# Kernel tuning notes

Hardware: AMD Instinct MI355X
Metric: run time of the kernel (lower is better)

## Reference

```python
import jax, jax.numpy as jnp
import numpy as np

EPS = 1e-5  # torch BatchNorm2d default eps
K = 3       # kernel_size
D = 1       # dilation (== padding)


def setup_inputs() -> dict:
    key = jax.random.key(0)
    k0, k1, k2 = jax.random.split(key, 3)
    N, C, H, W, O = 4, 2048, 32, 32, 256
    return {
        "x": jax.random.normal(k0, (N, C, H, W), jnp.float32),
        "conv_w": jax.random.normal(k1, (K * K, C, K, K), jnp.float32) * 0.01,
        "gamma": jnp.ones((K * K,), jnp.float32),
        "beta": jnp.zeros((K * K,), jnp.float32),
        "weight": jax.random.normal(k2, (O, C, K * K), jnp.float32) * 0.01,
    }


def reference(x, conv_w, gamma, beta, weight):
    n, c, h, w = x.shape
    # --- dynamic-kernel generator: conv (stride 1, pad=dilation) -> BN (train mode) -> softmax over K*K ---
    sigma = jax.lax.conv_general_dilated(
        x, conv_w, window_strides=(1, 1), padding=[(D, D), (D, D)],
        rhs_dilation=(D, D), dimension_numbers=("NCHW", "OIHW", "NCHW"))  # (n, K*K, h, w)
    mean = sigma.mean(axis=(0, 2, 3), keepdims=True)
    var = sigma.var(axis=(0, 2, 3), keepdims=True)  # biased variance, as torch BN uses for normalization
    sigma = (sigma - mean) * jax.lax.rsqrt(var + EPS)
    sigma = sigma * gamma[None, :, None, None] + beta[None, :, None, None]
    sigma = jax.nn.softmax(sigma, axis=1)            # softmax over the K*K kernel positions
    sigma = sigma.reshape(n, K * K, h * w)           # (n, K*K, h*w)
    # --- unfold (im2col), channel-major (C, kh, kw) ordering matching torch F.unfold ---
    patches = jax.lax.conv_general_dilated_patches(
        x, (K, K), (1, 1), [(D, D), (D, D)], rhs_dilation=(D, D),
        dimension_numbers=("NCHW", "OIHW", "NCHW"))  # (n, C*K*K, h, w)
    patches = patches.reshape(n, c, K * K, h * w)     # (n, C, K*K, h*w)
    # --- per-pixel dynamic weighting + learned projection ---
    # out[n,o,m] = sum_{c,l} patches[n,c,l,m] * sigma[n,l,m] * weight[o,c,l]
    out = jnp.einsum("nclm,nlm,ocl->nom", patches, sigma, weight)
    return out.reshape(n, weight.shape[0], h, w)
```

## Files before the change

kernel.cpp:

```cpp
#include <hip/hip_runtime.h>
#include <hip/hip_bf16.h>
#include <stdint.h>

typedef unsigned short u16;
typedef __attribute__((ext_vector_type(8))) short short8;
typedef __attribute__((ext_vector_type(4))) float floatx4;

#define N_IMG 4
#define C_IN  2048
#define HW    1024
#define KK    9
#define O_OUT 256
#define NPIX  4096
#define M_PAD  2560
#define H_ROWS 2432
#define K_DIM  2048
#define BN_EPS 1e-5f

#define OFF_A    0u
#define OFF_XT   10485760u
#define OFF_H    27262976u
#define OFF_SRAW 47185920u
#define OFF_STAT 47333376u

__device__ __forceinline__ u16 f2b(float f) {
    unsigned u = __float_as_uint(f);
    return (u16)((u + 0x7FFFu + ((u >> 16) & 1u)) >> 16);
}

__device__ __forceinline__ void load8f(const float* base, size_t eidx, u16* out) {
    const float* p = base + eidx;
    float4 a = ((const float4*)p)[0];
    float4 b = ((const float4*)p)[1];
    float f[8] = {a.x, a.y, a.z, a.w, b.x, b.y, b.z, b.w};
#pragma unroll
    for (int j = 0; j < 8; ++j) out[j] = f2b(f[j]);
}

__global__ void build_all(const float* __restrict__ x, const float* __restrict__ wgt,
                          const float* __restrict__ cw, u16* __restrict__ xt,
                          u16* __restrict__ A, float* __restrict__ stats) {
    __shared__ __align__(16) u16 lds[9 * 2056];
    int b = blockIdx.x, t = threadIdx.x;
    if (b < 2048) {
        int c0 = (b & 31) * 64, p0 = ((b >> 5) & 15) * 64, n = b >> 9;
        int rp = t >> 3;
        int pv = (t & 7) * 8;
        u16 h0[8], h1[8];
        load8f(x, (size_t)(n * C_IN + c0 + 2 * rp) * HW + p0 + pv, h0);
        load8f(x, (size_t)(n * C_IN + c0 + 2 * rp + 1) * HW + p0 + pv, h1);
        unsigned* l32 = (unsigned*)lds;
#pragma unroll
        for (int j = 0; j < 8; ++j)
            l32[(pv + j) * 35 + rp] = (unsigned)h0[j] | ((unsigned)h1[j] << 16);
        __syncthreads();
        int pr = t >> 3, cq = (t & 7) * 4;
        unsigned o0[4], o1[4];
#pragma unroll
        for (int i = 0; i < 4; ++i) {
            o0[i] = l32[pr * 35 + cq + i];
            o1[i] = l32[(pr + 32) * 35 + cq + i];
        }
        *(uint4*)(xt + (size_t)(n * HW + p0 + pr) * K_DIM + c0 + cq * 2) = *(uint4*)o0;
        *(uint4*)(xt + (size_t)(n * HW + p0 + pr + 32) * K_DIM + c0 + cq * 2) = *(uint4*)o1;
    } else if (b < 2304) {
        int o = b - 2048;
        size_t base = (size_t)o * 18432;
        for (int i = 0; i < 9; ++i) {
            int e0 = (t + i * 256) * 8;
            u16 hv[8];
            load8f(wgt, base + e0, hv);
#pragma unroll
            for (int j = 0; j < 8; ++j) {
                int e = e0 + j;
                int c = e / 9, l = e - c * 9;
                lds[l * 2056 + c] = hv[j];
            }
        }
        __syncthreads();
        for (int l = 0; l < 9; ++l) {
            size_t row = (size_t)l * 256 + o;
            *(uint4*)(A + row * K_DIM + t * 8) = *(const uint4*)&lds[l * 2056 + t * 8];
        }
    } else if (b < 2313) {
        int l = b - 2304;
        size_t base = (size_t)l * 18432;
        for (int i = 0; i < 9; ++i) {
            int e0 = (t + i * 256) * 8;
            u16 hv[8];
            load8f(cw, base + e0, hv);
#pragma unroll
            for (int j = 0; j < 8; ++j) {
                int e = e0 + j;
                int c = e / 9, k = e - c * 9;
                lds[k * 2056 + c] = hv[j];
            }
        }
        __syncthreads();
        for (int k = 0; k < 9; ++k) {
            size_t row = 2304 + (size_t)k * 9 + l;
            *(uint4*)(A + row * K_DIM + t * 8) = *(const uint4*)&lds[k * 2056 + t * 8];
        }
    } else {
        uint4 z = {0, 0, 0, 0};
        uint4* dst = (uint4*)(A + (size_t)2385 * K_DIM);
        for (int i = t; i < (47 * 2048) / 8; i += 256) dst[i] = z;
        if (t < 18) stats[t] = 0.0f;
    }
}

__device__ __forceinline__ void gload_lds16(const void* g, void* l) {
    __builtin_amdgcn_global_load_lds((__attribute__((address_space(1))) void*)(g),
                                     (__attribute__((address_space(3))) void*)(l), 16, 0, 0);
}

#define STG_A(bb, kt) do {                                                                   \
    gload_lds16(gA0 + (size_t)(w * 8) * K_DIM + (size_t)(kt) * 64,                           \
                As + (bb) * 10240 + w * 512);                                                \
    gload_lds16(gA0 + (size_t)((w + 8) * 8) * K_DIM + (size_t)(kt) * 64,                     \
                As + (bb) * 10240 + (w + 8) * 512);                                          \
    if (w < 4)                                                                               \
        gload_lds16(gA0 + (size_t)((w + 16) * 8) * K_DIM + (size_t)(kt) * 64,                \
                    As + (bb) * 10240 + (w + 16) * 512);                                     \
} while (0)

#define STG_B(bb, hh, kt) do {                                                               \
    gload_lds16(gB0 + (size_t)((hh) * 128 + (w * 2 + 0) * 8) * K_DIM + (size_t)(kt) * 64,    \
                Bs + (bb) * 16384 + (hh) * 8192 + w * 1024);                                 \
    gload_lds16(gB0 + (size_t)((hh) * 128 + (w * 2 + 1) * 8) * K_DIM + (size_t)(kt) * 64,    \
                Bs + (bb) * 16384 + (hh) * 8192 + w * 1024 + 512);                           \
} while (0)

#define RD_A(bb, mi, ks) (*(const short8*)(As + (bb) * 10240 + arow + (mi) * 1024 + col[ks]))
#define RD_B(bb, ni, ks) (*(const short8*)(Bs + (bb) * 16384 + brow + (ni) * 1024 + col[ks]))

#define READ_BALL(bb) do {                                                   \
    bq[0][0] = RD_B(bb, 0, 0); bq[1][0] = RD_B(bb, 1, 0);                    \
    bq[2][0] = RD_B(bb, 2, 0); bq[3][0] = RD_B(bb, 3, 0);                    \
    bq[0][1] = RD_B(bb, 0, 1); bq[1][1] = RD_B(bb, 1, 1);                    \
    bq[2][1] = RD_B(bb, 2, 1); bq[3][1] = RD_B(bb, 3, 1);                    \
} while (0)

#define READ_A2(bb, mlo, mhi) do {                                           \
    aq[0][0] = RD_A(bb, mlo, 0); aq[1][0] = RD_A(bb, mhi, 0);                \
    aq[0][1] = RD_A(bb, mlo, 1); aq[1][1] = RD_A(bb, mhi, 1);                \
} while (0)

#define READ_A1(bb, m) do {                                                  \
    aq[0][0] = RD_A(bb, m, 0); aq[0][1] = RD_A(bb, m, 1);                    \
} while (0)

#define MF(a, b, c) __builtin_amdgcn_mfma_f32_16x16x32_bf16(a, b, c, 0, 0, 0)

#define MFMA_PAIR(mlo, mhi) do {                                                             \
    acc[mlo][0] = MF(aq[0][0], bq[0][0], acc[mlo][0]); acc[mhi][0] = MF(aq[1][0], bq[0][0], acc[mhi][0]); \
    acc[mlo][1] = MF(aq[0][0], bq[1][0], acc[mlo][1]); acc[mhi][1] = MF(aq[1][0], bq[1][0], acc[mhi][1]); \
    acc[mlo][2] = MF(aq[0][0], bq[2][0], acc[mlo][2]); acc[mhi][2] = MF(aq[1][0], bq[2][0], acc[mhi][2]); \
    acc[mlo][3] = MF(aq[0][0], bq[3][0], acc[mlo][3]); acc[mhi][3] = MF(aq[1][0], bq[3][0], acc[mhi][3]); \
    acc[mlo][0] = MF(aq[0][1], bq[0][1], acc[mlo][0]); acc[mhi][0] = MF(aq[1][1], bq[0][1], acc[mhi][0]); \
    acc[mlo][1] = MF(aq[0][1], bq[1][1], acc[mlo][1]); acc[mhi][1] = MF(aq[1][1], bq[1][1], acc[mhi][1]); \
    acc[mlo][2] = MF(aq[0][1], bq[2][1], acc[mlo][2]); acc[mhi][2] = MF(aq[1][1], bq[2][1], acc[mhi][2]); \
    acc[mlo][3] = MF(aq[0][1], bq[3][1], acc[mlo][3]); acc[mhi][3] = MF(aq[1][1], bq[3][1], acc[mhi][3]); \
} while (0)

#define MFMA_ONE(m) do {                                                                     \
    acc[m][0] = MF(aq[0][0], bq[0][0], acc[m][0]); acc[m][1] = MF(aq[0][0], bq[1][0], acc[m][1]); \
    acc[m][2] = MF(aq[0][0], bq[2][0], acc[m][2]); acc[m][3] = MF(aq[0][0], bq[3][0], acc[m][3]); \
    acc[m][0] = MF(aq[0][1], bq[0][1], acc[m][0]); acc[m][1] = MF(aq[0][1], bq[1][1], acc[m][1]); \
    acc[m][2] = MF(aq[0][1], bq[2][1], acc[m][2]); acc[m][3] = MF(aq[0][1], bq[3][1], acc[m][3]); \
} while (0)

#define FENCE() asm volatile("" ::: "memory")
#define BARRIER() do { FENCE(); __builtin_amdgcn_s_barrier(); FENCE(); } while (0)

#define BAR1_PAIR(mlo, mhi) do {                             \
    BARRIER();                                               \
    __builtin_amdgcn_s_setprio(1);                           \
    MFMA_PAIR(mlo, mhi);                                     \
    __builtin_amdgcn_s_setprio(0);                           \
} while (0)
#define BAR1_ONE(m) do {                                     \
    BARRIER();                                               \
    __builtin_amdgcn_s_setprio(1);                           \
    MFMA_ONE(m);                                             \
    __builtin_amdgcn_s_setprio(0);                           \
} while (0)
#define VMW4() asm volatile("s_waitcnt vmcnt(4)" ::: "memory")
#define VMW0() asm volatile("s_waitcnt vmcnt(0)" ::: "memory")

__global__ __launch_bounds__(512, 2) void gemm_bt(const u16* __restrict__ A,
                                                  const u16* __restrict__ B,
                                                  __hip_bfloat16* __restrict__ C) {
    __shared__ __align__(16) u16 As[2 * 160 * 64];
    __shared__ __align__(16) u16 Bs[2 * 256 * 64];

    int orig = blockIdx.x;
    int wgid = (orig & 7) * 32 + (orig >> 3);
    int nt = wgid >> 4, mt = wgid & 15;
    int m0 = mt * 160, n0 = nt * 256;

    int t = threadIdx.x;
    int w = t >> 6, L = t & 63;
    int wm = w >> 2, wn = w & 3;
    int q = L >> 4, lm = L & 15;
    int lr = L >> 3, ls = L & 7;

    int csw = (ls ^ lr) * 8;
    const u16* gA0 = A + (size_t)(m0 + lr) * K_DIM + csw;
    const u16* gB0 = B + (size_t)(n0 + lr) * K_DIM + csw;

    int sw = (lm & 7) << 3;
    int arow = (wm * 80 + lm) * 64;
    int brow = (wn * 64 + lm) * 64;
    int col[2] = { (q * 8) ^ sw, (32 + q * 8) ^ sw };

    floatx4 acc[5][4];
    floatx4 z = {0.f, 0.f, 0.f, 0.f};
#pragma unroll
    for (int i = 0; i < 5; ++i)
#pragma unroll
        for (int j = 0; j < 4; ++j) acc[i][j] = z;

    short8 aq[2][2], bq[4][2];

    STG_A(0, 0);
    STG_B(0, 0, 0); STG_B(0, 1, 0);
    STG_B(1, 0, 1); STG_B(1, 1, 1);
    VMW4();
    BARRIER();

    for (int it = 0; it < 15; ++it) {
        int T = 2 * it;
        READ_A2(0, 0, 1); READ_BALL(0);
        STG_A(1, T + 1);
        BAR1_PAIR(0, 1);
        BARRIER();
        READ_A2(0, 2, 3);
        STG_B(0, 0, T + 2);
        BAR1_PAIR(2, 3);
        READ_A1(0, 4);
        STG_B(0, 1, T + 2);
        BAR1_ONE(4);
        VMW4(); BARRIER();
        READ_A2(1, 0, 1); READ_BALL(1);
        STG_A(0, T + 2);
        BAR1_PAIR(0, 1);
        BARRIER();
        READ_A2(1, 2, 3);
        STG_B(1, 0, T + 3);
        BAR1_PAIR(2, 3);
        READ_A1(1, 4);
        STG_B(1, 1, T + 3);
        BAR1_ONE(4);
        VMW4(); BARRIER();
    }

    READ_A2(0, 0, 1); READ_BALL(0);
    STG_A(1, 31);
    BAR1_PAIR(0, 1);
    READ_A2(0, 2, 3); BAR1_PAIR(2, 3);
    READ_A1(0, 4);    BAR1_ONE(4);
    VMW0(); BARRIER();
    READ_A2(1, 0, 1); READ_BALL(1); BAR1_PAIR(0, 1);
    READ_A2(1, 2, 3); BAR1_PAIR(2, 3);
    READ_A1(1, 4);    BAR1_ONE(4);

    if (m0 + 159 < H_ROWS) {
#pragma unroll
        for (int mi = 0; mi < 5; ++mi) {
            int gm = m0 + wm * 80 + mi * 16 + q * 4;
#pragma unroll
            for (int ni = 0; ni < 4; ++ni) {
                int gn = n0 + wn * 64 + ni * 16 + lm;
#pragma unroll
                for (int r = 0; r < 4; ++r)
                    C[(size_t)(gm + r) * NPIX + gn] = __float2bfloat16(acc[mi][ni][r]);
            }
        }
    } else {
#pragma unroll
        for (int mi = 0; mi < 5; ++mi) {
            int gm = m0 + wm * 80 + mi * 16 + q * 4;
#pragma unroll
            for (int ni = 0; ni < 4; ++ni) {
                int gn = n0 + wn * 64 + ni * 16 + lm;
#pragma unroll
                for (int r = 0; r < 4; ++r) {
                    int row = gm + r;
                    if (row < H_ROWS)
                        C[(size_t)row * NPIX + gn] = __float2bfloat16(acc[mi][ni][r]);
                }
            }
        }
    }
}

__global__ void sigma_stats(const __hip_bfloat16* __restrict__ Hm, float* __restrict__ sraw,
                            float* __restrict__ stats) {
    int b = blockIdx.x;
    int qq = b & 3, nl = b >> 2;
    int n = nl / 9, l = nl - n * 9;
    int t = threadIdx.x;
    int pix = qq * 256 + t;
    int y = pix >> 5, x = pix & 31;
    float v = 0.f;
#pragma unroll
    for (int k = 0; k < 9; ++k) {
        int yy = y + k / 3 - 1, xx = x + (k % 3) - 1;
        if (yy >= 0 && yy < 32 && xx >= 0 && xx < 32)
            v += __bfloat162float(Hm[(size_t)(2304 + k * 9 + l) * NPIX + n * HW + yy * 32 + xx]);
    }
    sraw[(size_t)nl * HW + pix] = v;
    __shared__ float r1[256], r2[256];
    r1[t] = v; r2[t] = v * v;
    __syncthreads();
    for (int s = 128; s > 0; s >>= 1) {
        if (t < s) { r1[t] += r1[t + s]; r2[t] += r2[t + s]; }
        __syncthreads();
    }
    if (t == 0) { atomicAdd(&stats[l], r1[0]); atomicAdd(&stats[9 + l], r2[0]); }
}

__global__ void tail(const __hip_bfloat16* __restrict__ Hm, const float* __restrict__ sraw,
                     const float* __restrict__ stats, const float* __restrict__ gamma,
                     const float* __restrict__ beta, float* __restrict__ out) {
    int b = blockIdx.x;
    int n = b >> 8, rem = b & 255;
    int ph = rem >> 7, og = rem & 127;
    int t = threadIdx.x;
    float mean[9], istd[9], gg[9], bb[9];
#pragma unroll
    for (int l = 0; l < 9; ++l) {
        float m = stats[l] * (1.f / 4096.f);
        float var = stats[9 + l] * (1.f / 4096.f) - m * m;
        mean[l] = m; istd[l] = rsqrtf(var + BN_EPS);
        gg[l] = gamma[l]; bb[l] = beta[l];
    }
    const __hip_bfloat16* hb = Hm + (size_t)(og * 2) * NPIX + (size_t)n * HW;
    float* ob = out + ((size_t)n * 256 + og * 2) * HW;
#pragma unroll
    for (int i = 0; i < 2; ++i) {
        int pix = ph * 512 + i * 256 + t;
        int y = pix >> 5, x = pix & 31;
        float v[9];
        float mx = -1e30f;
#pragma unroll
        for (int l = 0; l < 9; ++l) {
            float tv = (sraw[(size_t)(n * 9 + l) * HW + pix] - mean[l]) * istd[l];
            tv = tv * gg[l] + bb[l];
            v[l] = tv; mx = fmaxf(mx, tv);
        }
        float ssum = 0.f;
#pragma unroll
        for (int l = 0; l < 9; ++l) { v[l] = __expf(v[l] - mx); ssum += v[l]; }
        float inv = 1.f / ssum;
        float acc0 = 0.f, acc1 = 0.f;
#pragma unroll
        for (int l = 0; l < 9; ++l) {
            int dy = l / 3 - 1, dx = l % 3 - 1;
            int yy = y + dy, xx = x + dx;
            if (yy >= 0 && yy < 32 && xx >= 0 && xx < 32) {
                float sv = v[l] * inv;
                size_t hidx = (size_t)(l * 256) * NPIX + (size_t)(pix + dy * 32 + dx);
                acc0 += sv * __bfloat162float(hb[hidx]);
                acc1 += sv * __bfloat162float(hb[hidx + NPIX]);
            }
        }
        ob[pix] = acc0;
        ob[HW + pix] = acc1;
    }
}

extern "C" void kernel_launch(void* const* d_in, const int* in_sizes, int n_in,
                              void* d_out, int out_size, void* d_ws, size_t ws_size,
                              hipStream_t stream) {
    const float* x     = (const float*)d_in[0];
    const float* cw    = (const float*)d_in[1];
    const float* gamma = (const float*)d_in[2];
    const float* beta  = (const float*)d_in[3];
    const float* wgt   = (const float*)d_in[4];

    char* ws = (char*)d_ws;
    u16*   Abuf = (u16*)(ws + OFF_A);
    u16*   XT   = (u16*)(ws + OFF_XT);
    u16*   Hm   = (u16*)(ws + OFF_H);
    float* sraw = (float*)(ws + OFF_SRAW);
    float* stats= (float*)(ws + OFF_STAT);

    build_all<<<2314, 256, 0, stream>>>(x, wgt, cw, XT, Abuf, stats);
    gemm_bt<<<256, 512, 0, stream>>>(Abuf, XT, (__hip_bfloat16*)Hm);
    sigma_stats<<<N_IMG * KK * 4, 256, 0, stream>>>((const __hip_bfloat16*)Hm, sraw, stats);
    tail<<<1024, 256, 0, stream>>>((const __hip_bfloat16*)Hm, sraw, stats, gamma, beta, (float*)d_out);
}
```

Measured before the change: 159.8 us.

## Software-pipeline LDS fragment reads ahead of MFMA groups in GEMM main loop

Restructures the GEMM inner loop so that LDS fragment reads for the next MFMA group are issued before the current group's MFMAs. The MFMA work is regrouped into three phases (a 2x2 block, a cross block, and the rest) that reuse fragments already in registers. The next tile's first fragments are prefetched into a double-buffered register set before the buffer flip. This is meant to hide LDS read latency behind matrix work, at the cost of more live VGPRs and changed waitcnt/barrier placement (vmcnt(2) instead of vmcnt(4)).

```diff
diff --git a/kernel.cpp b/kernel.cpp
--- a/kernel.cpp
+++ b/kernel.cpp
@@ -134,57 +134,66 @@
 #define RD_A(bb, mi, ks) (*(const short8*)(As + (bb) * 10240 + arow + (mi) * 1024 + col[ks]))
 #define RD_B(bb, ni, ks) (*(const short8*)(Bs + (bb) * 16384 + brow + (ni) * 1024 + col[ks]))
 
-#define READ_BALL(bb) do {                                                   \
-    bq[0][0] = RD_B(bb, 0, 0); bq[1][0] = RD_B(bb, 1, 0);                    \
-    bq[2][0] = RD_B(bb, 2, 0); bq[3][0] = RD_B(bb, 3, 0);                    \
-    bq[0][1] = RD_B(bb, 0, 1); bq[1][1] = RD_B(bb, 1, 1);                    \
-    bq[2][1] = RD_B(bb, 2, 1); bq[3][1] = RD_B(bb, 3, 1);                    \
-} while (0)
-
-#define READ_A2(bb, mlo, mhi) do {                                           \
-    aq[0][0] = RD_A(bb, mlo, 0); aq[1][0] = RD_A(bb, mhi, 0);                \
-    aq[0][1] = RD_A(bb, mlo, 1); aq[1][1] = RD_A(bb, mhi, 1);                \
-} while (0)
-
-#define READ_A1(bb, m) do {                                                  \
-    aq[0][0] = RD_A(bb, m, 0); aq[0][1] = RD_A(bb, m, 1);                    \
+#define PRE_S0(par, bb) do {                                                 \
+    s0A[par][0][0] = RD_A(bb, 0, 0); s0A[par][1][0] = RD_A(bb, 1, 0);        \
+    s0B[par][0][0] = RD_B(bb, 0, 0); s0B[par][1][0] = RD_B(bb, 1, 0);        \
+    s0A[par][0][1] = RD_A(bb, 0, 1); s0A[par][1][1] = RD_A(bb, 1, 1);        \
+    s0B[par][0][1] = RD_B(bb, 0, 1); s0B[par][1][1] = RD_B(bb, 1, 1);        \
+} while (0)
+
+#define PRE_S1(bb) do {                                                      \
+    s1A[0][0] = RD_A(bb, 2, 0); s1A[1][0] = RD_A(bb, 3, 0);                  \
+    s1B[0][0] = RD_B(bb, 2, 0); s1B[1][0] = RD_B(bb, 3, 0);                  \
+    s1A[0][1] = RD_A(bb, 2, 1); s1A[1][1] = RD_A(bb, 3, 1);                  \
+    s1B[0][1] = RD_B(bb, 2, 1); s1B[1][1] = RD_B(bb, 3, 1);                  \
+} while (0)
+
+#define PRE_S2(bb) do {                                                      \
+    s2A[0] = RD_A(bb, 4, 0); s2A[1] = RD_A(bb, 4, 1);                        \
 } while (0)
 
 #define MF(a, b, c) __builtin_amdgcn_mfma_f32_16x16x32_bf16(a, b, c, 0, 0, 0)
 
-#define MFMA_PAIR(mlo, mhi) do {                                                             \
-    acc[mlo][0] = MF(aq[0][0], bq[0][0], acc[mlo][0]); acc[mhi][0] = MF(aq[1][0], bq[0][0], acc[mhi][0]); \
-    acc[mlo][1] = MF(aq[0][0], bq[1][0], acc[mlo][1]); acc[mhi][1] = MF(aq[1][0], bq[1][0], acc[mhi][1]); \
-    acc[mlo][2] = MF(aq[0][0], bq[2][0], acc[mlo][2]); acc[mhi][2] = MF(aq[1][0], bq[2][0], acc[mhi][2]); \
-    acc[mlo][3] = MF(aq[0][0], bq[3][0], acc[mlo][3]); acc[mhi][3] = MF(aq[1][0], bq[3][0], acc[mhi][3]); \
-    acc[mlo][0] = MF(aq[0][1], bq[0][1], acc[mlo][0]); acc[mhi][0] = MF(aq[1][1], bq[0][1], acc[mhi][0]); \
-    acc[mlo][1] = MF(aq[0][1], bq[1][1], acc[mlo][1]); acc[mhi][1] = MF(aq[1][1], bq[1][1], acc[mhi][1]); \
-    acc[mlo][2] = MF(aq[0][1], bq[2][1], acc[mlo][2]); acc[mhi][2] = MF(aq[1][1], bq[2][1], acc[mhi][2]); \
-    acc[mlo][3] = MF(aq[0][1], bq[3][1], acc[mlo][3]); acc[mhi][3] = MF(aq[1][1], bq[3][1], acc[mhi][3]); \
-} while (0)
-
-#define MFMA_ONE(m) do {                                                                     \
-    acc[m][0] = MF(aq[0][0], bq[0][0], acc[m][0]); acc[m][1] = MF(aq[0][0], bq[1][0], acc[m][1]); \
-    acc[m][2] = MF(aq[0][0], bq[2][0], acc[m][2]); acc[m][3] = MF(aq[0][0], bq[3][0], acc[m][3]); \
-    acc[m][0] = MF(aq[0][1], bq[0][1], acc[m][0]); acc[m][1] = MF(aq[0][1], bq[1][1], acc[m][1]); \
-    acc[m][2] = MF(aq[0][1], bq[2][1], acc[m][2]); acc[m][3] = MF(aq[0][1], bq[3][1], acc[m][3]); \
-} while (0)
+#define G0K(par, k) do {                                                     \
+    acc[0][0] = MF(s0A[par][0][k], s0B[par][0][k], acc[0][0]);               \
+    acc[0][1] = MF(s0A[par][0][k], s0B[par][1][k], acc[0][1]);               \
+    acc[1][0] = MF(s0A[par][1][k], s0B[par][0][k], acc[1][0]);               \
+    acc[1][1] = MF(s0A[par][1][k], s0B[par][1][k], acc[1][1]);               \
+} while (0)
+#define G0(par) do { G0K(par, 0); G0K(par, 1); } while (0)
+
+#define G1K(par, k) do {                                                     \
+    acc[0][2] = MF(s0A[par][0][k], s1B[0][k], acc[0][2]);                    \
+    acc[0][3] = MF(s0A[par][0][k], s1B[1][k], acc[0][3]);                    \
+    acc[1][2] = MF(s0A[par][1][k], s1B[0][k], acc[1][2]);                    \
+    acc[1][3] = MF(s0A[par][1][k], s1B[1][k], acc[1][3]);                    \
+    acc[2][0] = MF(s1A[0][k], s0B[par][0][k], acc[2][0]);                    \
+    acc[2][1] = MF(s1A[0][k], s0B[par][1][k], acc[2][1]);                    \
+    acc[3][0] = MF(s1A[1][k], s0B[par][0][k], acc[3][0]);                    \
+    acc[3][1] = MF(s1A[1][k], s0B[par][1][k], acc[3][1]);                    \
+} while (0)
+#define G1(par) do { G1K(par, 0); G1K(par, 1); } while (0)
+
+#define G2K(par, k) do {                                                     \
+    acc[2][2] = MF(s1A[0][k], s1B[0][k], acc[2][2]);                         \
+    acc[2][3] = MF(s1A[0][k], s1B[1][k], acc[2][3]);                         \
+    acc[3][2] = MF(s1A[1][k], s1B[0][k], acc[3][2]);                         \
+    acc[3][3] = MF(s1A[1][k], s1B[1][k], acc[3][3]);                         \
+    acc[4][0] = MF(s2A[k], s0B[par][0][k], acc[4][0]);                       \
+    acc[4][1] = MF(s2A[k], s0B[par][1][k], acc[4][1]);                       \
+    acc[4][2] = MF(s2A[k], s1B[0][k], acc[4][2]);                           \
+    acc[4][3] = MF(s2A[k], s1B[1][k], acc[4][3]);                           \
+} while (0)
+#define G2(par) do { G2K(par, 0); G2K(par, 1); } while (0)
 
 #define FENCE() asm volatile("" ::: "memory")
 #define BARRIER() do { FENCE(); __builtin_amdgcn_s_barrier(); FENCE(); } while (0)
-
-#define BAR1_PAIR(mlo, mhi) do {                             \
-    BARRIER();                                               \
+#define PRIO_MFMA(GRP) do {                                  \
     __builtin_amdgcn_s_setprio(1);                           \
-    MFMA_PAIR(mlo, mhi);                                     \
+    GRP;                                                     \
     __builtin_amdgcn_s_setprio(0);                           \
 } while (0)
-#define BAR1_ONE(m) do {                                     \
-    BARRIER();                                               \
-    __builtin_amdgcn_s_setprio(1);                           \
-    MFMA_ONE(m);                                             \
-    __builtin_amdgcn_s_setprio(0);                           \
-} while (0)
+#define VMW2() asm volatile("s_waitcnt vmcnt(2)" ::: "memory")
 #define VMW4() asm volatile("s_waitcnt vmcnt(4)" ::: "memory")
 #define VMW0() asm volatile("s_waitcnt vmcnt(0)" ::: "memory")
 
@@ -221,49 +230,63 @@
 #pragma unroll
         for (int j = 0; j < 4; ++j) acc[i][j] = z;
 
-    short8 aq[2][2], bq[4][2];
+    short8 s0A[2][2][2], s0B[2][2][2];
+    short8 s1A[2][2], s1B[2][2];
+    short8 s2A[2];
 
     STG_A(0, 0);
     STG_B(0, 0, 0); STG_B(0, 1, 0);
     STG_B(1, 0, 1); STG_B(1, 1, 1);
     VMW4();
     BARRIER();
+    PRE_S0(0, 0);
 
     for (int it = 0; it < 15; ++it) {
         int T = 2 * it;
-        READ_A2(0, 0, 1); READ_BALL(0);
+        BARRIER();
+        PRE_S1(0);
         STG_A(1, T + 1);
-        BAR1_PAIR(0, 1);
+        PRIO_MFMA(G0(0));
         BARRIER();
-        READ_A2(0, 2, 3);
+        PRE_S2(0);
         STG_B(0, 0, T + 2);
-        BAR1_PAIR(2, 3);
-        READ_A1(0, 4);
+        PRIO_MFMA(G1(0));
+        VMW2(); BARRIER();
+        PRE_S0(1, 1);
         STG_B(0, 1, T + 2);
-        BAR1_ONE(4);
-        VMW4(); BARRIER();
-        READ_A2(1, 0, 1); READ_BALL(1);
+        PRIO_MFMA(G2(0));
+        BARRIER();
+        PRE_S1(1);
         STG_A(0, T + 2);
-        BAR1_PAIR(0, 1);
+        PRIO_MFMA(G0(1));
         BARRIER();
-        READ_A2(1, 2, 3);
+        PRE_S2(1);
         STG_B(1, 0, T + 3);
-        BAR1_PAIR(2, 3);
-        READ_A1(1, 4);
+        PRIO_MFMA(G1(1));
+        VMW2(); BARRIER();
+        PRE_S0(0, 0);
         STG_B(1, 1, T + 3);
-        BAR1_ONE(4);
-        VMW4(); BARRIER();
-    }
-
-    READ_A2(0, 0, 1); READ_BALL(0);
+        PRIO_MFMA(G2(1));
+    }
+
+    BARRIER();
+    PRE_S1(0);
     STG_A(1, 31);
-    BAR1_PAIR(0, 1);
-    READ_A2(0, 2, 3); BAR1_PAIR(2, 3);
-    READ_A1(0, 4);    BAR1_ONE(4);
+    PRIO_MFMA(G0(0));
+    BARRIER();
+    PRE_S2(0);
+    PRIO_MFMA(G1(0));
     VMW0(); BARRIER();
-    READ_A2(1, 0, 1); READ_BALL(1); BAR1_PAIR(0, 1);
-    READ_A2(1, 2, 3); BAR1_PAIR(2, 3);
-    READ_A1(1, 4);    BAR1_ONE(4);
+    PRE_S0(1, 1);
+    PRIO_MFMA(G2(0));
+    BARRIER();
+    PRE_S1(1);
+    PRIO_MFMA(G0(1));
+    BARRIER();
+    PRE_S2(1);
+    PRIO_MFMA(G1(1));
+    BARRIER();
+    PRIO_MFMA(G2(1));
 
     if (m0 + 159 < H_ROWS) {
 #pragma unroll
```

After: 162.6 us. Within noise of the previous version (+1.8%).

## Load GEMM A operand directly from global into registers, bypassing LDS

Applied to the files above, without the earlier changes.

Drops the LDS staging buffer for the A tile. Each wave now loads its own A fragments from global memory straight into a double-buffered register array, while B is still staged through LDS. The per-k-step schedule is cut from several barrier-separated MFMA groups to one compute block per buffer. This removes LDS traffic and barriers for A, but raises register pressure (20 extra short8 per thread) under launch bounds of 512 threads at 2 blocks per SM. It also relies on uncoalesced, duplicated global reads of A across waves that share the same rows.

```diff
diff --git a/kernel.cpp b/kernel.cpp
--- a/kernel.cpp
+++ b/kernel.cpp
@@ -114,16 +114,6 @@
                                      (__attribute__((address_space(3))) void*)(l), 16, 0, 0);
 }
 
-#define STG_A(bb, kt) do {                                                                   \
-    gload_lds16(gA0 + (size_t)(w * 8) * K_DIM + (size_t)(kt) * 64,                           \
-                As + (bb) * 10240 + w * 512);                                                \
-    gload_lds16(gA0 + (size_t)((w + 8) * 8) * K_DIM + (size_t)(kt) * 64,                     \
-                As + (bb) * 10240 + (w + 8) * 512);                                          \
-    if (w < 4)                                                                               \
-        gload_lds16(gA0 + (size_t)((w + 16) * 8) * K_DIM + (size_t)(kt) * 64,                \
-                    As + (bb) * 10240 + (w + 16) * 512);                                     \
-} while (0)
-
 #define STG_B(bb, hh, kt) do {                                                               \
     gload_lds16(gB0 + (size_t)((hh) * 128 + (w * 2 + 0) * 8) * K_DIM + (size_t)(kt) * 64,    \
                 Bs + (bb) * 16384 + (hh) * 8192 + w * 1024);                                 \
@@ -131,67 +121,38 @@
                 Bs + (bb) * 16384 + (hh) * 8192 + w * 1024 + 512);                           \
 } while (0)
 
-#define RD_A(bb, mi, ks) (*(const short8*)(As + (bb) * 10240 + arow + (mi) * 1024 + col[ks]))
 #define RD_B(bb, ni, ks) (*(const short8*)(Bs + (bb) * 16384 + brow + (ni) * 1024 + col[ks]))
 
-#define READ_BALL(bb) do {                                                   \
-    bq[0][0] = RD_B(bb, 0, 0); bq[1][0] = RD_B(bb, 1, 0);                    \
-    bq[2][0] = RD_B(bb, 2, 0); bq[3][0] = RD_B(bb, 3, 0);                    \
-    bq[0][1] = RD_B(bb, 0, 1); bq[1][1] = RD_B(bb, 1, 1);                    \
-    bq[2][1] = RD_B(bb, 2, 1); bq[3][1] = RD_B(bb, 3, 1);                    \
+#define LD_A(par, kt) do {                                                                   \
+    _Pragma("unroll") for (int mi_ = 0; mi_ < 5; ++mi_)                                      \
+    _Pragma("unroll") for (int ks_ = 0; ks_ < 2; ++ks_)                                      \
+        aR[par][mi_][ks_] = *(const short8*)(gA + (size_t)(mi_ * 16) * K_DIM                 \
+                                             + (size_t)(kt) * 64 + ks_ * 32);                \
 } while (0)
 
-#define READ_A2(bb, mlo, mhi) do {                                           \
-    aq[0][0] = RD_A(bb, mlo, 0); aq[1][0] = RD_A(bb, mhi, 0);                \
-    aq[0][1] = RD_A(bb, mlo, 1); aq[1][1] = RD_A(bb, mhi, 1);                \
-} while (0)
-
-#define READ_A1(bb, m) do {                                                  \
-    aq[0][0] = RD_A(bb, m, 0); aq[0][1] = RD_A(bb, m, 1);                    \
-} while (0)
-
 #define MF(a, b, c) __builtin_amdgcn_mfma_f32_16x16x32_bf16(a, b, c, 0, 0, 0)
 
-#define MFMA_PAIR(mlo, mhi) do {                                                             \
-    acc[mlo][0] = MF(aq[0][0], bq[0][0], acc[mlo][0]); acc[mhi][0] = MF(aq[1][0], bq[0][0], acc[mhi][0]); \
-    acc[mlo][1] = MF(aq[0][0], bq[1][0], acc[mlo][1]); acc[mhi][1] = MF(aq[1][0], bq[1][0], acc[mhi][1]); \
-    acc[mlo][2] = MF(aq[0][0], bq[2][0], acc[mlo][2]); acc[mhi][2] = MF(aq[1][0], bq[2][0], acc[mhi][2]); \
-    acc[mlo][3] = MF(aq[0][0], bq[3][0], acc[mlo][3]); acc[mhi][3] = MF(aq[1][0], bq[3][0], acc[mhi][3]); \
-    acc[mlo][0] = MF(aq[0][1], bq[0][1], acc[mlo][0]); acc[mhi][0] = MF(aq[1][1], bq[0][1], acc[mhi][0]); \
-    acc[mlo][1] = MF(aq[0][1], bq[1][1], acc[mlo][1]); acc[mhi][1] = MF(aq[1][1], bq[1][1], acc[mhi][1]); \
-    acc[mlo][2] = MF(aq[0][1], bq[2][1], acc[mlo][2]); acc[mhi][2] = MF(aq[1][1], bq[2][1], acc[mhi][2]); \
-    acc[mlo][3] = MF(aq[0][1], bq[3][1], acc[mlo][3]); acc[mhi][3] = MF(aq[1][1], bq[3][1], acc[mhi][3]); \
-} while (0)
-
-#define MFMA_ONE(m) do {                                                                     \
-    acc[m][0] = MF(aq[0][0], bq[0][0], acc[m][0]); acc[m][1] = MF(aq[0][0], bq[1][0], acc[m][1]); \
-    acc[m][2] = MF(aq[0][0], bq[2][0], acc[m][2]); acc[m][3] = MF(aq[0][0], bq[3][0], acc[m][3]); \
-    acc[m][0] = MF(aq[0][1], bq[0][1], acc[m][0]); acc[m][1] = MF(aq[0][1], bq[1][1], acc[m][1]); \
-    acc[m][2] = MF(aq[0][1], bq[2][1], acc[m][2]); acc[m][3] = MF(aq[0][1], bq[3][1], acc[m][3]); \
+#define COMPUTE(par) do {                                                                    \
+    bq[0][0] = RD_B(par, 0, 0); bq[1][0] = RD_B(par, 1, 0);                                  \
+    bq[2][0] = RD_B(par, 2, 0); bq[3][0] = RD_B(par, 3, 0);                                  \
+    bq[0][1] = RD_B(par, 0, 1); bq[1][1] = RD_B(par, 1, 1);                                  \
+    bq[2][1] = RD_B(par, 2, 1); bq[3][1] = RD_B(par, 3, 1);                                  \
+    __builtin_amdgcn_s_setprio(1);                                                           \
+    _Pragma("unroll") for (int ks_ = 0; ks_ < 2; ++ks_)                                      \
+      _Pragma("unroll") for (int mi_ = 0; mi_ < 5; ++mi_)                                    \
+        _Pragma("unroll") for (int ni_ = 0; ni_ < 4; ++ni_)                                  \
+          acc[mi_][ni_] = MF(aR[par][mi_][ks_], bq[ni_][ks_], acc[mi_][ni_]);                \
+    __builtin_amdgcn_s_setprio(0);                                                           \
 } while (0)
 
 #define FENCE() asm volatile("" ::: "memory")
 #define BARRIER() do { FENCE(); __builtin_amdgcn_s_barrier(); FENCE(); } while (0)
-
-#define BAR1_PAIR(mlo, mhi) do {                             \
-    BARRIER();                                               \
-    __builtin_amdgcn_s_setprio(1);                           \
-    MFMA_PAIR(mlo, mhi);                                     \
-    __builtin_amdgcn_s_setprio(0);                           \
-} while (0)
-#define BAR1_ONE(m) do {                                     \
-    BARRIER();                                               \
-    __builtin_amdgcn_s_setprio(1);                           \
-    MFMA_ONE(m);                                             \
-    __builtin_amdgcn_s_setprio(0);                           \
-} while (0)
-#define VMW4() asm volatile("s_waitcnt vmcnt(4)" ::: "memory")
-#define VMW0() asm volatile("s_waitcnt vmcnt(0)" ::: "memory")
+#define VMW14() asm volatile("s_waitcnt vmcnt(14)" ::: "memory")
+#define VMW0()  asm volatile("s_waitcnt vmcnt(0)" ::: "memory")
 
 __global__ __launch_bounds__(512, 2) void gemm_bt(const u16* __restrict__ A,
                                                   const u16* __restrict__ B,
                                                   __hip_bfloat16* __restrict__ C) {
-    __shared__ __align__(16) u16 As[2 * 160 * 64];
     __shared__ __align__(16) u16 Bs[2 * 256 * 64];
 
     int orig = blockIdx.x;
@@ -206,11 +167,10 @@
     int lr = L >> 3, ls = L & 7;
 
     int csw = (ls ^ lr) * 8;
-    const u16* gA0 = A + (size_t)(m0 + lr) * K_DIM + csw;
     const u16* gB0 = B + (size_t)(n0 + lr) * K_DIM + csw;
+    const u16* gA = A + (size_t)(m0 + wm * 80 + lm) * K_DIM + q * 8;
 
     int sw = (lm & 7) << 3;
-    int arow = (wm * 80 + lm) * 64;
     int brow = (wn * 64 + lm) * 64;
     int col[2] = { (q * 8) ^ sw, (32 + q * 8) ^ sw };
 
@@ -221,49 +181,35 @@
 #pragma unroll
         for (int j = 0; j < 4; ++j) acc[i][j] = z;
 
-    short8 aq[2][2], bq[4][2];
-
-    STG_A(0, 0);
+    short8 aR[2][5][2];
+    short8 bq[4][2];
+
+    LD_A(0, 0);
     STG_B(0, 0, 0); STG_B(0, 1, 0);
     STG_B(1, 0, 1); STG_B(1, 1, 1);
-    VMW4();
+    LD_A(1, 1);
+    VMW14();
     BARRIER();
 
     for (int it = 0; it < 15; ++it) {
         int T = 2 * it;
-        READ_A2(0, 0, 1); READ_BALL(0);
-        STG_A(1, T + 1);
-        BAR1_PAIR(0, 1);
+        COMPUTE(0);
         BARRIER();
-        READ_A2(0, 2, 3);
-        STG_B(0, 0, T + 2);
-        BAR1_PAIR(2, 3);
-        READ_A1(0, 4);
-        STG_B(0, 1, T + 2);
-        BAR1_ONE(4);
-        VMW4(); BARRIER();
-        READ_A2(1, 0, 1); READ_BALL(1);
-        STG_A(0, T + 2);
-        BAR1_PAIR(0, 1);
+        STG_B(0, 0, T + 2); STG_B(0, 1, T + 2);
+        LD_A(0, T + 2);
+        VMW14();
         BARRIER();
-        READ_A2(1, 2, 3);
-        STG_B(1, 0, T + 3);
-        BAR1_PAIR(2, 3);
-        READ_A1(1, 4);
-        STG_B(1, 1, T + 3);
-        BAR1_ONE(4);
-        VMW4(); BARRIER();
-    }
-
-    READ_A2(0, 0, 1); READ_BALL(0);
-    STG_A(1, 31);
-    BAR1_PAIR(0, 1);
-    READ_A2(0, 2, 3); BAR1_PAIR(2, 3);
-    READ_A1(0, 4);    BAR1_ONE(4);
+        COMPUTE(1);
+        BARRIER();
+        STG_B(1, 0, T + 3); STG_B(1, 1, T + 3);
+        LD_A(1, T + 3);
+        VMW14();
+        BARRIER();
+    }
+
+    COMPUTE(0);
     VMW0(); BARRIER();
-    READ_A2(1, 0, 1); READ_BALL(1); BAR1_PAIR(0, 1);
-    READ_A2(1, 2, 3); BAR1_PAIR(2, 3);
-    READ_A1(1, 4);    BAR1_ONE(4);
+    COMPUTE(1);
 
     if (m0 + 159 < H_ROWS) {
 #pragma unroll
```

Result: slower. 211.3 us (+32.2%).
